# Optimization experiments

Measured on AMD Instinct MI355X. Metric: run time of the kernel, lower is better.

Reference implementation:

```python
import jax, jax.numpy as jnp
import numpy as np

N_NODES = 50000
N_EDGES = 1600000
IN_DIM = 128
N_HEADS = 8
OUT_DIM = 16
LEAKY_SLOPE = 0.2


def setup_inputs() -> dict:
    key = jax.random.key(0)
    k1, k2, k3, k4, k5, k6 = jax.random.split(key, 6)
    x = jax.random.normal(k1, (N_NODES, IN_DIM), dtype=jnp.float32)
    W = jax.random.normal(k2, (N_HEADS * OUT_DIM, IN_DIM), dtype=jnp.float32) * (1.414 / np.sqrt(IN_DIM))
    attn_l = jax.random.normal(k3, (N_HEADS, OUT_DIM), dtype=jnp.float32) * 0.5
    attn_r = jax.random.normal(k4, (N_HEADS, OUT_DIM), dtype=jnp.float32) * 0.5
    src = jax.random.randint(k5, (N_EDGES,), 0, N_NODES, dtype=jnp.int64) if jax.config.jax_enable_x64 else jax.random.randint(k5, (N_EDGES,), 0, N_NODES, dtype=jnp.int32)
    dst = jax.random.randint(k6, (N_EDGES,), 0, N_NODES, dtype=src.dtype)
    return {"x": x, "W": W, "attn_l": attn_l, "attn_r": attn_r, "src": src, "dst": dst}


def reference(x, W, attn_l, attn_r, src, dst):
    n = x.shape[0]
    # fc projection -> [N, H, D]
    ft = (x @ W.T).reshape(n, N_HEADS, OUT_DIM)
    # per-node attention logits (bmm with [H,D,1] vector == contraction over D) -> [N, H]
    a1 = jnp.einsum('nhd,hd->nh', ft, attn_l)
    a2 = jnp.einsum('nhd,hd->nh', ft, attn_r)
    # per-edge score: leaky_relu(a1[src] + a2[dst]) -> [E, H]
    e = jax.nn.leaky_relu(a1[src] + a2[dst], negative_slope=LEAKY_SLOPE)
    # segment softmax over incoming edges of each dst node (numerically stable)
    seg_max = jax.ops.segment_max(e, dst, num_segments=n)          # [N, H]
    seg_max = jnp.where(jnp.isfinite(seg_max), seg_max, 0.0)       # isolated nodes -> 0
    e_exp = jnp.exp(e - seg_max[dst])                              # [E, H]
    denom = jax.ops.segment_sum(e_exp, dst, num_segments=n)        # [N, H]
    alpha = e_exp / denom[dst]                                     # [E, H]
    # weighted scatter-sum of src messages -> [N, H, D]
    msgs = ft[src] * alpha[:, :, None]                             # [E, H, D]
    out = jax.ops.segment_sum(msgs, dst, num_segments=n)
    return out
```

## Files before the change

kernel.cpp:

```cpp
#include <hip/hip_runtime.h>
#include <math.h>

#define N_NODES 50000
#define N_EDGES 1600000
#define IN_DIM 128
#define N_HEADS 8
#define OUT_DIM 16
#define HD 128
#define DEG_CAP 128
#define NBUCK 196
#define BCAP 12288
#define CHUNK 2048
#define BIN_BLOCKS ((N_EDGES + CHUNK - 1) / CHUNK)
#define PBLK ((N_NODES + 31) / 32)

__device__ __forceinline__ unsigned short f2bf(float f) {
    union { float f; unsigned int u; } v; v.f = f;
    unsigned int u = v.u;
    unsigned int r = (u + 0x7fffu + ((u >> 16) & 1u)) >> 16;
    return (unsigned short)r;
}

__global__ void k_transpose_w(const float* __restrict__ W, float* __restrict__ Wt,
                              int* __restrict__ bucket_cnt, int* __restrict__ ovf_cnt) {
    if (blockIdx.x == 0) {
        int t = threadIdx.x;
        if (t < NBUCK) bucket_cnt[t] = 0;
        if (t == 0) *ovf_cnt = 0;
    }
    int flat4 = blockIdx.x * blockDim.x + threadIdx.x;
    if (flat4 >= (HD * IN_DIM) / 4) return;
    int c  = flat4 >> 5;
    int k4 = flat4 & 31;
    float4 v = ((const float4*)W)[flat4];
    int k = k4 * 4;
    Wt[(k + 0) * HD + c] = v.x;
    Wt[(k + 1) * HD + c] = v.y;
    Wt[(k + 2) * HD + c] = v.z;
    Wt[(k + 3) * HD + c] = v.w;
}

__global__ __launch_bounds__(256) void k_proj_bin(
    const float* __restrict__ x, const float* __restrict__ Wt,
    const float* __restrict__ attn_l, const float* __restrict__ attn_r,
    unsigned short* __restrict__ ftb, float* __restrict__ a1, float* __restrict__ a2,
    const int* __restrict__ src, const int* __restrict__ dst,
    unsigned int* __restrict__ region, int* __restrict__ bucket_cnt,
    int* __restrict__ ovf_cnt, unsigned int* __restrict__ ovf) {
    __shared__ __align__(16) char smem[13312];
    int tid = threadIdx.x;

    if (blockIdx.x < PBLK) {
        float (*red_l)[32] = (float(*)[32])smem;
        float (*red_r)[32] = (float(*)[32])(smem + 4096);

        int cb = (tid & 31) * 4;
        int nb = (tid >> 5) * 4;
        int node0 = blockIdx.x * 32;

        float4 acc[4];
        acc[0] = acc[1] = acc[2] = acc[3] = make_float4(0.f, 0.f, 0.f, 0.f);

        const float* xrow[4];
#pragma unroll
        for (int i = 0; i < 4; i++) {
            int n = node0 + nb + i;
            if (n >= N_NODES) n = N_NODES - 1;
            xrow[i] = x + (size_t)n * IN_DIM;
        }

        for (int k = 0; k < IN_DIM; k += 4) {
            float4 w0 = *(const float4*)(Wt + (k + 0) * HD + cb);
            float4 w1 = *(const float4*)(Wt + (k + 1) * HD + cb);
            float4 w2 = *(const float4*)(Wt + (k + 2) * HD + cb);
            float4 w3 = *(const float4*)(Wt + (k + 3) * HD + cb);
#pragma unroll
            for (int i = 0; i < 4; i++) {
                float4 xv = *(const float4*)(xrow[i] + k);
                acc[i].x = fmaf(xv.w, w3.x, fmaf(xv.z, w2.x, fmaf(xv.y, w1.x, fmaf(xv.x, w0.x, acc[i].x))));
                acc[i].y = fmaf(xv.w, w3.y, fmaf(xv.z, w2.y, fmaf(xv.y, w1.y, fmaf(xv.x, w0.y, acc[i].y))));
                acc[i].z = fmaf(xv.w, w3.z, fmaf(xv.z, w2.z, fmaf(xv.y, w1.z, fmaf(xv.x, w0.z, acc[i].z))));
                acc[i].w = fmaf(xv.w, w3.w, fmaf(xv.z, w2.w, fmaf(xv.y, w1.w, fmaf(xv.x, w0.w, acc[i].w))));
            }
        }

#pragma unroll
        for (int i = 0; i < 4; i++) {
            int n = node0 + nb + i;
            if (n < N_NODES) {
                ushort4 us;
                us.x = f2bf(acc[i].x); us.y = f2bf(acc[i].y);
                us.z = f2bf(acc[i].z); us.w = f2bf(acc[i].w);
                *(ushort4*)(ftb + (size_t)n * HD + cb) = us;
            }
        }

        int h   = cb >> 4;
        int sub = cb & 15;
        float4 al = *(const float4*)(attn_l + h * OUT_DIM + sub);
        float4 ar = *(const float4*)(attn_r + h * OUT_DIM + sub);
        int col = (h << 2) | (sub >> 2);
#pragma unroll
        for (int i = 0; i < 4; i++) {
            float pl = acc[i].x * al.x + acc[i].y * al.y + acc[i].z * al.z + acc[i].w * al.w;
            float pr = acc[i].x * ar.x + acc[i].y * ar.y + acc[i].z * ar.z + acc[i].w * ar.w;
            red_l[nb + i][col] = pl;
            red_r[nb + i][col] = pr;
        }
        __syncthreads();
        int nl = tid >> 3, hh = tid & 7;
        int n = node0 + nl;
        if (n < N_NODES) {
            float s1 = red_l[nl][hh * 4 + 0] + red_l[nl][hh * 4 + 1] + red_l[nl][hh * 4 + 2] + red_l[nl][hh * 4 + 3];
            float s2 = red_r[nl][hh * 4 + 0] + red_r[nl][hh * 4 + 1] + red_r[nl][hh * 4 + 2] + red_r[nl][hh * 4 + 3];
            a1[n * N_HEADS + hh] = s1;
            a2[n * N_HEADS + hh] = s2;
        }
    } else {
        unsigned int* stage = (unsigned int*)smem;
        int* hist  = (int*)(smem + 8192);
        int* scan  = (int*)(smem + 9216);
        int* loff  = (int*)(smem + 10240);
        int* lcur  = (int*)(smem + 11264);
        int* rbase = (int*)(smem + 12288);

        int t = tid;
        int base = (blockIdx.x - PBLK) * CHUNK;
        int nvalid = min(CHUNK, N_EDGES - base);

        hist[t] = 0;
        __syncthreads();

        unsigned int mypack[CHUNK / 256];
#pragma unroll
        for (int k = 0; k < CHUNK / 256; k++) {
            int i = t + k * 256;
            if (i < nvalid) {
                int s = src[base + i];
                int d = dst[base + i];
                unsigned int p = ((unsigned int)d << 16) | (unsigned int)s;
                mypack[k] = p;
                atomicAdd(&hist[d >> 8], 1);
            }
        }
        __syncthreads();
        int h = hist[t];
        scan[t] = h;
        __syncthreads();
        for (int d2 = 1; d2 < 256; d2 <<= 1) {
            int u = (t >= d2) ? scan[t - d2] : 0;
            __syncthreads();
            scan[t] += u;
            __syncthreads();
        }
        int excl = scan[t] - h;
        loff[t] = excl;
        lcur[t] = excl;
        rbase[t] = (t < NBUCK && h > 0) ? atomicAdd(&bucket_cnt[t], h) : 0;
        __syncthreads();
#pragma unroll
        for (int k = 0; k < CHUNK / 256; k++) {
            int i = t + k * 256;
            if (i < nvalid) {
                unsigned int p = mypack[k];
                int slot = atomicAdd(&lcur[p >> 24], 1);
                stage[slot] = p;
            }
        }
        __syncthreads();
        for (int i = t; i < nvalid; i += 256) {
            unsigned int p = stage[i];
            int b = p >> 24;
            int pos = rbase[b] + (i - loff[b]);
            if (pos < BCAP) region[(size_t)b * BCAP + pos] = p;
            else { int o = atomicAdd(ovf_cnt, 1); ovf[o] = p; }
        }
    }
}

__global__ __launch_bounds__(512) void k_place(
    const unsigned int* __restrict__ region, const int* __restrict__ bucket_cnt,
    const int* __restrict__ ovf_cnt, const unsigned int* __restrict__ ovf,
    int* __restrict__ offs, int* __restrict__ esrc) {
    int b = blockIdx.x;
    int t = threadIdx.x;
    __shared__ int sb[256];
    __shared__ int hist[256], s[256], curs[256];

    if (t < 256) {
        sb[t] = (t < NBUCK) ? bucket_cnt[t] : 0;
        hist[t] = 0;
    }
    __syncthreads();
    for (int d = 1; d < 256; d <<= 1) {
        int u = (t >= d && t < 256) ? sb[t - d] : 0;
        __syncthreads();
        if (t < 256) sb[t] += u;
        __syncthreads();
    }
    int truec = bucket_cnt[b];
    int base_b = sb[b] - truec;
    int rc = min(truec, BCAP);
    const unsigned int* reg = region + (size_t)b * BCAP;

    for (int i = t; i < rc; i += 512) atomicAdd(&hist[(reg[i] >> 16) & 255], 1);
    int no = 0;
    if (truec > BCAP) {
        no = *ovf_cnt;
        for (int i = t; i < no; i += 512)
            if ((int)(ovf[i] >> 24) == b) atomicAdd(&hist[(ovf[i] >> 16) & 255], 1);
    }
    __syncthreads();
    int h = (t < 256) ? hist[t] : 0;
    if (t < 256) s[t] = h;
    __syncthreads();
    for (int d = 1; d < 256; d <<= 1) {
        int u = (t >= d && t < 256) ? s[t - d] : 0;
        __syncthreads();
        if (t < 256) s[t] += u;
        __syncthreads();
    }
    if (t < 256) {
        int pos0 = base_b + s[t] - h;
        int node = b * 256 + t;
        if (node < N_NODES) offs[node] = pos0;
        curs[t] = pos0;
    }
    if (b == NBUCK - 1 && t == 0) offs[N_NODES] = N_EDGES;
    __syncthreads();
    for (int i = t; i < rc; i += 512) {
        unsigned int p = reg[i];
        int pos = atomicAdd(&curs[(p >> 16) & 255], 1);
        esrc[pos] = (int)(p & 0xffffu);
    }
    if (truec > BCAP) {
        for (int i = t; i < no; i += 512) {
            unsigned int p = ovf[i];
            if ((int)(p >> 24) == b) {
                int pos = atomicAdd(&curs[(p >> 16) & 255], 1);
                esrc[pos] = (int)(p & 0xffffu);
            }
        }
    }
}

__global__ __launch_bounds__(256) void k_aggregate(
    const unsigned short* __restrict__ ftb, const float* __restrict__ a1,
    const float* __restrict__ a2, const int* __restrict__ offs,
    const int* __restrict__ esrc, float* __restrict__ out) {
    __shared__ float lw[4][DEG_CAP * N_HEADS];
    __shared__ int   ls[4][DEG_CAP];

    int wid  = threadIdx.x >> 6;
    int lane = threadIdx.x & 63;
    int node = blockIdx.x * 4 + wid;
    float* w  = lw[wid];
    int*   si = ls[wid];

    int off = offs[node];
    int deg = offs[node + 1] - off;

    int h1 = lane & 7;
    int es = lane >> 3;
    float a2h = a2[node * N_HEADS + h1];

    float l = 0.f;
    for (int base = 0; base < deg; base += 8) {
        int e = base + es;
        if (e < deg) {
            int s = esrc[off + e];
            float t = a1[s * N_HEADS + h1] + a2h;
            t = t > 0.f ? t : 0.2f * t;
            float ww = __expf(t);
            l += ww;
            if (e < DEG_CAP) {
                w[e * N_HEADS + h1] = ww;
                if (h1 == 0) si[e] = s;
            }
        }
    }
    l += __shfl_xor(l, 8);
    l += __shfl_xor(l, 16);
    l += __shfl_xor(l, 32);
    float invl = (deg > 0) ? 1.f / l : 0.f;

    int lim = min(deg, DEG_CAP);
    for (int e = es; e < lim; e += 8) w[e * N_HEADS + h1] *= invl;

    int hl = lane >> 3;
    float invl2 = __shfl(invl, hl);
    float a2h2  = __shfl(a2h, hl);

    float accx = 0.f, accy = 0.f;
#pragma unroll 8
    for (int j = 0; j < lim; j++) {
        float ww = w[j * N_HEADS + hl];
        int s = si[j];
        unsigned int p = *(const unsigned int*)(ftb + (size_t)s * HD + lane * 2);
        float fx = __uint_as_float(p << 16);
        float fy = __uint_as_float(p & 0xffff0000u);
        accx = fmaf(ww, fx, accx);
        accy = fmaf(ww, fy, accy);
    }
    for (int j = DEG_CAP; j < deg; j++) {
        int s = esrc[off + j];
        float t = a1[s * N_HEADS + hl] + a2h2;
        t = t > 0.f ? t : 0.2f * t;
        float ww = __expf(t) * invl2;
        unsigned int p = *(const unsigned int*)(ftb + (size_t)s * HD + lane * 2);
        accx = fmaf(ww, __uint_as_float(p << 16), accx);
        accy = fmaf(ww, __uint_as_float(p & 0xffff0000u), accy);
    }

    float2 o; o.x = accx; o.y = accy;
    *(float2*)(out + (size_t)node * HD + lane * 2) = o;
}

extern "C" void kernel_launch(void* const* d_in, const int* in_sizes, int n_in,
                              void* d_out, int out_size, void* d_ws, size_t ws_size,
                              hipStream_t stream) {
    const float* x      = (const float*)d_in[0];
    const float* W      = (const float*)d_in[1];
    const float* attn_l = (const float*)d_in[2];
    const float* attn_r = (const float*)d_in[3];
    const int*   src    = (const int*)d_in[4];
    const int*   dst    = (const int*)d_in[5];
    float* out = (float*)d_out;

    char* ws = (char*)d_ws;
    size_t o = 0;
    auto alloc = [&](size_t bytes) -> char* {
        char* p = ws + o;
        o = (o + bytes + 255) & ~(size_t)255;
        return p;
    };
    unsigned short* ftb = (unsigned short*)alloc((size_t)N_NODES * HD * 2);
    float* a1          = (float*)alloc((size_t)N_NODES * N_HEADS * 4);
    float* a2          = (float*)alloc((size_t)N_NODES * N_HEADS * 4);
    float* Wt          = (float*)alloc((size_t)HD * IN_DIM * 4);
    unsigned int* region = (unsigned int*)alloc((size_t)NBUCK * BCAP * 4);
    int* bucket_cnt    = (int*)alloc((size_t)NBUCK * 4);
    int* ovf_cnt       = (int*)alloc(4);
    unsigned int* ovf  = (unsigned int*)alloc((size_t)N_EDGES * 4);
    int* offs          = (int*)alloc((size_t)(N_NODES + 1) * 4);
    int* esrc          = (int*)alloc((size_t)N_EDGES * 4);

    (void)in_sizes; (void)n_in; (void)out_size; (void)ws_size;

    k_transpose_w<<<16, 256, 0, stream>>>(W, Wt, bucket_cnt, ovf_cnt);
    k_proj_bin<<<PBLK + BIN_BLOCKS, 256, 0, stream>>>(
        x, Wt, attn_l, attn_r, ftb, a1, a2,
        src, dst, region, bucket_cnt, ovf_cnt, ovf);
    k_place<<<NBUCK, 512, 0, stream>>>(region, bucket_cnt, ovf_cnt, ovf, offs, esrc);
    k_aggregate<<<N_NODES / 4, 256, 0, stream>>>(ftb, a1, a2, offs, esrc, out);
}
```

Before: 233.1 us.

## Use finer 64-node buckets for edge binning and restructure bucket scans

Destination bucketing goes from 196 buckets of 256 nodes to 784 buckets of 64 nodes, with a larger edge chunk per bin block and a new shared multi-element exclusive scan over all buckets. Each k_place block now handles a smaller bucket with 256 threads, so the placement work is spread over more, lighter blocks and uses a short 64-entry scan. The projection kernel gets occupancy hints and partial unrolling. The risk is more global atomics on bucket counters and more shared memory per bin block.

```diff
diff --git a/kernel.cpp b/kernel.cpp
--- a/kernel.cpp
+++ b/kernel.cpp
@@ -8,9 +8,9 @@
 #define OUT_DIM 16
 #define HD 128
 #define DEG_CAP 128
-#define NBUCK 196
-#define BCAP 12288
-#define CHUNK 2048
+#define NBUCK 784
+#define BCAP 2560
+#define CHUNK 4096
 #define BIN_BLOCKS ((N_EDGES + CHUNK - 1) / CHUNK)
 #define PBLK ((N_NODES + 31) / 32)
 
@@ -21,18 +21,40 @@
     return (unsigned short)r;
 }
 
+__device__ __forceinline__ void scan_nbuck_excl(int* arr, int* part) {
+    int t = threadIdx.x;
+    int v0 = 0, v1 = 0, v2 = 0, v3 = 0, cs = 0;
+    if (t < NBUCK / 4) {
+        v0 = arr[4 * t]; v1 = arr[4 * t + 1]; v2 = arr[4 * t + 2]; v3 = arr[4 * t + 3];
+        cs = v0 + v1 + v2 + v3;
+    }
+    part[t] = cs;
+    __syncthreads();
+    for (int d = 1; d < 256; d <<= 1) {
+        int u = (t >= d) ? part[t - d] : 0;
+        __syncthreads();
+        part[t] += u;
+        __syncthreads();
+    }
+    if (t < NBUCK / 4) {
+        int run = part[t] - cs;
+        arr[4 * t] = run; run += v0;
+        arr[4 * t + 1] = run; run += v1;
+        arr[4 * t + 2] = run; run += v2;
+        arr[4 * t + 3] = run;
+    }
+    __syncthreads();
+}
+
 __global__ void k_transpose_w(const float* __restrict__ W, float* __restrict__ Wt,
                               int* __restrict__ bucket_cnt, int* __restrict__ ovf_cnt) {
-    if (blockIdx.x == 0) {
-        int t = threadIdx.x;
-        if (t < NBUCK) bucket_cnt[t] = 0;
-        if (t == 0) *ovf_cnt = 0;
-    }
-    int flat4 = blockIdx.x * blockDim.x + threadIdx.x;
-    if (flat4 >= (HD * IN_DIM) / 4) return;
-    int c  = flat4 >> 5;
-    int k4 = flat4 & 31;
-    float4 v = ((const float4*)W)[flat4];
+    int g = blockIdx.x * 256 + threadIdx.x;
+    if (g < NBUCK) bucket_cnt[g] = 0;
+    if (g == 0) *ovf_cnt = 0;
+    if (g >= (HD * IN_DIM) / 4) return;
+    int c  = g >> 5;
+    int k4 = g & 31;
+    float4 v = ((const float4*)W)[g];
     int k = k4 * 4;
     Wt[(k + 0) * HD + c] = v.x;
     Wt[(k + 1) * HD + c] = v.y;
@@ -40,14 +62,14 @@
     Wt[(k + 3) * HD + c] = v.w;
 }
 
-__global__ __launch_bounds__(256) void k_proj_bin(
+__global__ __launch_bounds__(256, 2) void k_proj_bin(
     const float* __restrict__ x, const float* __restrict__ Wt,
     const float* __restrict__ attn_l, const float* __restrict__ attn_r,
     unsigned short* __restrict__ ftb, float* __restrict__ a1, float* __restrict__ a2,
     const int* __restrict__ src, const int* __restrict__ dst,
     unsigned int* __restrict__ region, int* __restrict__ bucket_cnt,
     int* __restrict__ ovf_cnt, unsigned int* __restrict__ ovf) {
-    __shared__ __align__(16) char smem[13312];
+    __shared__ __align__(16) char smem[23680];
     int tid = threadIdx.x;
 
     if (blockIdx.x < PBLK) {
@@ -69,6 +91,7 @@
             xrow[i] = x + (size_t)n * IN_DIM;
         }
 
+#pragma unroll 2
         for (int k = 0; k < IN_DIM; k += 4) {
             float4 w0 = *(const float4*)(Wt + (k + 0) * HD + cb);
             float4 w1 = *(const float4*)(Wt + (k + 1) * HD + cb);
@@ -118,17 +141,15 @@
         }
     } else {
         unsigned int* stage = (unsigned int*)smem;
-        int* hist  = (int*)(smem + 8192);
-        int* scan  = (int*)(smem + 9216);
-        int* loff  = (int*)(smem + 10240);
-        int* lcur  = (int*)(smem + 11264);
-        int* rbase = (int*)(smem + 12288);
+        int* hist  = (int*)(smem + 16384);
+        int* delta = (int*)(smem + 19520);
+        int* part  = (int*)(smem + 22656);
 
         int t = tid;
         int base = (blockIdx.x - PBLK) * CHUNK;
         int nvalid = min(CHUNK, N_EDGES - base);
 
-        hist[t] = 0;
+        for (int i = t; i < NBUCK; i += 256) hist[i] = 0;
         __syncthreads();
 
         unsigned int mypack[CHUNK / 256];
@@ -140,104 +161,92 @@
                 int d = dst[base + i];
                 unsigned int p = ((unsigned int)d << 16) | (unsigned int)s;
                 mypack[k] = p;
-                atomicAdd(&hist[d >> 8], 1);
-            }
-        }
-        __syncthreads();
-        int h = hist[t];
-        scan[t] = h;
-        __syncthreads();
-        for (int d2 = 1; d2 < 256; d2 <<= 1) {
-            int u = (t >= d2) ? scan[t - d2] : 0;
-            __syncthreads();
-            scan[t] += u;
-            __syncthreads();
-        }
-        int excl = scan[t] - h;
-        loff[t] = excl;
-        lcur[t] = excl;
-        rbase[t] = (t < NBUCK && h > 0) ? atomicAdd(&bucket_cnt[t], h) : 0;
+                atomicAdd(&hist[d >> 6], 1);
+            }
+        }
+        __syncthreads();
+        for (int i = t; i < NBUCK; i += 256) {
+            int h = hist[i];
+            delta[i] = (h > 0) ? atomicAdd(&bucket_cnt[i], h) : 0;
+        }
+        __syncthreads();
+        scan_nbuck_excl(hist, part);
+        for (int i = t; i < NBUCK; i += 256) delta[i] -= hist[i];
         __syncthreads();
 #pragma unroll
         for (int k = 0; k < CHUNK / 256; k++) {
             int i = t + k * 256;
             if (i < nvalid) {
                 unsigned int p = mypack[k];
-                int slot = atomicAdd(&lcur[p >> 24], 1);
+                int slot = atomicAdd(&hist[p >> 22], 1);
                 stage[slot] = p;
             }
         }
         __syncthreads();
         for (int i = t; i < nvalid; i += 256) {
             unsigned int p = stage[i];
-            int b = p >> 24;
-            int pos = rbase[b] + (i - loff[b]);
+            int b = p >> 22;
+            int pos = delta[b] + i;
             if (pos < BCAP) region[(size_t)b * BCAP + pos] = p;
             else { int o = atomicAdd(ovf_cnt, 1); ovf[o] = p; }
         }
     }
 }
 
-__global__ __launch_bounds__(512) void k_place(
+__global__ __launch_bounds__(256) void k_place(
     const unsigned int* __restrict__ region, const int* __restrict__ bucket_cnt,
     const int* __restrict__ ovf_cnt, const unsigned int* __restrict__ ovf,
     int* __restrict__ offs, int* __restrict__ esrc) {
     int b = blockIdx.x;
     int t = threadIdx.x;
-    __shared__ int sb[256];
-    __shared__ int hist[256], s[256], curs[256];
-
-    if (t < 256) {
-        sb[t] = (t < NBUCK) ? bucket_cnt[t] : 0;
-        hist[t] = 0;
-    }
-    __syncthreads();
-    for (int d = 1; d < 256; d <<= 1) {
-        int u = (t >= d && t < 256) ? sb[t - d] : 0;
-        __syncthreads();
-        if (t < 256) sb[t] += u;
-        __syncthreads();
-    }
+    __shared__ int sb[NBUCK], part[256];
+    __shared__ int hist[64], sc[64], curs[64];
+
+    for (int i = t; i < NBUCK; i += 256) sb[i] = bucket_cnt[i];
+    if (t < 64) hist[t] = 0;
+    __syncthreads();
+    scan_nbuck_excl(sb, part);
+
     int truec = bucket_cnt[b];
-    int base_b = sb[b] - truec;
+    int base_b = sb[b];
     int rc = min(truec, BCAP);
     const unsigned int* reg = region + (size_t)b * BCAP;
 
-    for (int i = t; i < rc; i += 512) atomicAdd(&hist[(reg[i] >> 16) & 255], 1);
+    for (int i = t; i < rc; i += 256) atomicAdd(&hist[(reg[i] >> 16) & 63], 1);
     int no = 0;
     if (truec > BCAP) {
         no = *ovf_cnt;
-        for (int i = t; i < no; i += 512)
-            if ((int)(ovf[i] >> 24) == b) atomicAdd(&hist[(ovf[i] >> 16) & 255], 1);
-    }
-    __syncthreads();
-    int h = (t < 256) ? hist[t] : 0;
-    if (t < 256) s[t] = h;
-    __syncthreads();
-    for (int d = 1; d < 256; d <<= 1) {
-        int u = (t >= d && t < 256) ? s[t - d] : 0;
-        __syncthreads();
-        if (t < 256) s[t] += u;
-        __syncthreads();
-    }
-    if (t < 256) {
-        int pos0 = base_b + s[t] - h;
-        int node = b * 256 + t;
+        for (int i = t; i < no; i += 256)
+            if ((int)(ovf[i] >> 22) == b) atomicAdd(&hist[(ovf[i] >> 16) & 63], 1);
+    }
+    __syncthreads();
+    int h = (t < 64) ? hist[t] : 0;
+    if (t < 64) sc[t] = h;
+    __syncthreads();
+    for (int d = 1; d < 64; d <<= 1) {
+        int u = (t >= d && t < 64) ? sc[t - d] : 0;
+        __syncthreads();
+        if (t < 64) sc[t] += u;
+        __syncthreads();
+    }
+    if (t < 64) {
+        int pos0 = base_b + sc[t] - h;
+        int node = b * 64 + t;
         if (node < N_NODES) offs[node] = pos0;
         curs[t] = pos0;
     }
-    if (b == NBUCK - 1 && t == 0) offs[N_NODES] = N_EDGES;
-    __syncthreads();
-    for (int i = t; i < rc; i += 512) {
+    if (b == 0 && t == 0) offs[N_NODES] = N_EDGES;
+    __syncthreads();
+    for (int i = t; i < rc; i += 256) {
         unsigned int p = reg[i];
-        int pos = atomicAdd(&curs[(p >> 16) & 255], 1);
+        int pos = atomicAdd(&curs[(p >> 16) & 63], 1);
         esrc[pos] = (int)(p & 0xffffu);
     }
     if (truec > BCAP) {
-        for (int i = t; i < no; i += 512) {
+        for (int i = t; i < no; i += 256) {
             unsigned int p = ovf[i];
-            if ((int)(p >> 24) == b) {
-                int pos = atomicAdd(&curs[(p >> 16) & 255], 1);
+            if ((int)(p >> 22) == b) {
+                int pos = atomicAdd(&curs[(p >> 16) & 63], 1);
                 esrc[pos] = (int)(p & 0xffffu);
             }
         }
@@ -351,6 +360,6 @@
     k_proj_bin<<<PBLK + BIN_BLOCKS, 256, 0, stream>>>(
         x, Wt, attn_l, attn_r, ftb, a1, a2,
         src, dst, region, bucket_cnt, ovf_cnt, ovf);
-    k_place<<<NBUCK, 512, 0, stream>>>(region, bucket_cnt, ovf_cnt, ovf, offs, esrc);
+    k_place<<<NBUCK, 256, 0, stream>>>(region, bucket_cnt, ovf_cnt, ovf, offs, esrc);
     k_aggregate<<<N_NODES / 4, 256, 0, stream>>>(ftb, a1, a2, offs, esrc, out);
 }
```

New measurement: 229.4 us. No clear change (-1.6%).
